# Kernel optimization log

Measured on AMD Instinct MI355X. Metric: run time of the kernel, lower is better.

The kernel has to match this reference:

```python
import jax, jax.numpy as jnp
import numpy as np

B, L, D, H = 2, 2048, 1024, 16
HD = D // H  # head_dim = 64


def setup_inputs() -> dict:
    key = jax.random.key(0)
    ks = jax.random.split(key, 8)
    queries = jax.random.normal(ks[0], (B, L, D), dtype=jnp.float32)
    keys = jax.random.normal(ks[1], (B, L, D), dtype=jnp.float32)
    values = jax.random.normal(ks[2], (B, L, D), dtype=jnp.float32)
    mask = jax.random.randint(ks[3], (B, L, L), 0, 2) > 0  # True = masked
    s = 1.0 / np.sqrt(D)
    W_q = jax.random.normal(ks[4], (D, D), dtype=jnp.float32) * s
    W_k = jax.random.normal(ks[5], (D, D), dtype=jnp.float32) * s
    W_v = jax.random.normal(ks[6], (D, D), dtype=jnp.float32) * s
    W_o = jax.random.normal(ks[7], (D, D), dtype=jnp.float32) * s
    return {"queries": queries, "keys": keys, "values": values,
            "W_q": W_q, "W_k": W_k, "W_v": W_v, "W_o": W_o, "mask": mask}


def _split_heads(x):
    # [B, L, D] -> [B, H, L, HD]
    return x.reshape(B, L, H, HD).transpose(0, 2, 1, 3)


def reference(queries, keys, values, W_q, W_k, W_v, W_o, mask):
    # Linear projections (nn.Linear: x @ W.T, no bias)
    q = _split_heads(queries @ W_q.T)   # [B,H,Lq,HD]
    k = _split_heads(keys @ W_k.T)      # [B,H,Lk,HD]
    v = _split_heads(values @ W_v.T)    # [B,H,Lk,HD]
    scores = jnp.einsum('bnqd,bnkd->bnqk', q, k) / np.sqrt(HD)
    scores = jnp.where(mask[:, None, :, :], -1e9, scores)
    attn = jax.nn.softmax(scores, axis=-1)
    ctx = jnp.einsum('bnqk,bnkd->bnqd', attn, v)
    ctx = ctx.transpose(0, 2, 1, 3).reshape(B, L, D)
    return ctx @ W_o.T  # dropout p=0.0 -> identity
```

## Files before the change

kernel.cpp:

```cpp
#include <hip/hip_runtime.h>
#include <hip/hip_bf16.h>

typedef __bf16 bf16;
typedef __attribute__((ext_vector_type(8))) __bf16 bf16x8;
typedef __attribute__((ext_vector_type(4))) __bf16 bf16x4;
typedef __attribute__((ext_vector_type(4))) float f32x4;

#define B_   2
#define L_   2048
#define D_   1024
#define H_   16
#define HD_  64

__device__ __forceinline__ float fast_exp2(float x) {
  float e; asm("v_exp_f32 %0, %1" : "=v"(e) : "v"(x)); return e;
}

__device__ __forceinline__ void gll16(const bf16* g, bf16* l) {
  __builtin_amdgcn_global_load_lds((const __attribute__((address_space(1))) void*)g,
                                   (__attribute__((address_space(3))) void*)l,
                                   16, 0, 0);
}

__global__ void detect_kernel(const unsigned short* __restrict__ q_u,
                              const unsigned char* __restrict__ m_u,
                              int* __restrict__ flags) {
  __shared__ int cnt, odd;
  if (threadIdx.x == 0) { cnt = 0; odd = 0; }
  __syncthreads();
  int c = 0, o = 0;
  for (int i = 0; i < 8; i++) {
    int idx = threadIdx.x * 8 + i;
    unsigned e = (q_u[idx] >> 7) & 0xFF;
    if (e >= 0x8F || (e > 0 && e <= 0x6F)) c++;
    if ((idx & 3) && m_u[idx]) o = 1;
  }
  atomicAdd(&cnt, c);
  if (o) atomicOr(&odd, 1);
  __syncthreads();
  if (threadIdx.x == 0) { flags[0] = (cnt > 128) ? 1 : 0; flags[1] = odd; }
}

__device__ __forceinline__ void canon_body(const void* src, bf16* dst, int i, int f) {
  if (f) {
    const float4* s = (const float4*)src;
    float4 a = s[i / 4], b2 = s[i / 4 + 1];
    bf16x8 o;
    o[0] = (bf16)a.x;  o[1] = (bf16)a.y;  o[2] = (bf16)a.z;  o[3] = (bf16)a.w;
    o[4] = (bf16)b2.x; o[5] = (bf16)b2.y; o[6] = (bf16)b2.z; o[7] = (bf16)b2.w;
    *(bf16x8*)(dst + i) = o;
  } else {
    *(bf16x8*)(dst + i) = ((const bf16x8*)src)[i / 8];
  }
}

__global__ __launch_bounds__(256) void canon_pack(
    const void* xq, const void* xk, const void* xv,
    const void* Wq, const void* Wk, const void* Wv, const void* Wo,
    const void* mp,
    bf16* cxq, bf16* cxk, bf16* cxv,
    bf16* cWq, bf16* cWk, bf16* cWv, bf16* cWo,
    unsigned* __restrict__ bitsT,
    const int* __restrict__ flags) {
  int t = blockIdx.x;
  if (t >= 8192) {
    int wid = (t - 8192) * 256 + threadIdx.x;
    unsigned v = 0;
    if (flags[1]) {
      const uchar4* p = (const uchar4*)mp;
#pragma unroll
      for (int c = 0; c < 8; c++) {
        uchar4 u = p[wid * 8 + c];
        v |= (u.x ? 1u : 0u) << (c * 4 + 0);
        v |= (u.y ? 1u : 0u) << (c * 4 + 1);
        v |= (u.z ? 1u : 0u) << (c * 4 + 2);
        v |= (u.w ? 1u : 0u) << (c * 4 + 3);
      }
    } else {
      const int4* p = (const int4*)mp;
#pragma unroll
      for (int c = 0; c < 8; c++) {
        int4 u = p[wid * 8 + c];
        v |= (u.x ? 1u : 0u) << (c * 4 + 0);
        v |= (u.y ? 1u : 0u) << (c * 4 + 1);
        v |= (u.z ? 1u : 0u) << (c * 4 + 2);
        v |= (u.w ? 1u : 0u) << (c * 4 + 3);
      }
    }
    int row = wid >> 6, word = wid & 63;
    int kt = word >> 1, half = word & 1;
    bitsT[((size_t)kt * 4096 + row) * 2 + half] = v;
    return;
  }
  const int f = flags[0];
  const void* src; bf16* dst; int base;
  if (t < 2048)      { src = xq; dst = cxq; base = t * 2048; }
  else if (t < 4096) { src = xk; dst = cxk; base = (t - 2048) * 2048; }
  else if (t < 6144) { src = xv; dst = cxv; base = (t - 4096) * 2048; }
  else {
    int w = t - 6144, wi = w >> 9;
    base = (w & 511) * 2048;
    if (wi == 0)      { src = Wq; dst = cWq; }
    else if (wi == 1) { src = Wk; dst = cWk; }
    else if (wi == 2) { src = Wv; dst = cWv; }
    else              { src = Wo; dst = cWo; }
  }
  canon_body(src, dst, base + threadIdx.x * 8, f);
}

__global__ __launch_bounds__(256) void gemm_qkv(
    const bf16* __restrict__ Aq, const bf16* __restrict__ Bq, bf16* __restrict__ Cq,
    const bf16* __restrict__ Ak, const bf16* __restrict__ Bk, bf16* __restrict__ Ck,
    const bf16* __restrict__ Av, const bf16* __restrict__ Bv, bf16* __restrict__ VT) {
  __shared__ bf16 smem[128 * 136];
  bf16* sA = smem;
  bf16* sB = smem + 4096;
  const int z = blockIdx.z;
  const bf16* A  = (z == 0) ? Aq : (z == 1) ? Ak : Av;
  const bf16* Bm = (z == 0) ? Bq : (z == 1) ? Bk : Bv;

  const int tid = threadIdx.x;
  const int w = tid >> 6, lane = tid & 63, qd = lane >> 4, r = lane & 15;
  const int wm = w >> 1, wn = w & 1;
  const int m0 = blockIdx.x * 128, n0 = blockIdx.y * 128;

  f32x4 acc[4][4];
#pragma unroll
  for (int i = 0; i < 4; i++)
#pragma unroll
    for (int j = 0; j < 4; j++) acc[i][j] = (f32x4){0.f, 0.f, 0.f, 0.f};

  for (int k0 = 0; k0 < 1024; k0 += 32) {
    __syncthreads();
#pragma unroll
    for (int p = 0; p < 2; p++) {
      int c = p * 256 + tid;
      gll16(A + (size_t)(m0 + (c >> 2)) * 1024 + k0 + (c & 3) * 8, sA + c * 8);
    }
#pragma unroll
    for (int p = 0; p < 2; p++) {
      int c = p * 256 + tid;
      gll16(Bm + (size_t)(n0 + (c >> 2)) * 1024 + k0 + (c & 3) * 8, sB + c * 8);
    }
    __syncthreads();
    bf16x8 af[4], bfv[4];
#pragma unroll
    for (int i = 0; i < 4; i++)
      af[i] = *(const bf16x8*)&sA[(wm * 64 + i * 16 + r) * 32 + qd * 8];
#pragma unroll
    for (int j = 0; j < 4; j++)
      bfv[j] = *(const bf16x8*)&sB[(wn * 64 + j * 16 + r) * 32 + qd * 8];
#pragma unroll
    for (int i = 0; i < 4; i++)
#pragma unroll
      for (int j = 0; j < 4; j++)
        acc[i][j] = __builtin_amdgcn_mfma_f32_16x16x32_bf16(af[i], bfv[j], acc[i][j], 0, 0, 0);
  }

  if (z < 2) {
    bf16* C = (z == 0) ? Cq : Ck;
    const float s = (z == 0) ? 0.1803368801f : 1.0f;
#pragma unroll
    for (int i = 0; i < 4; i++)
#pragma unroll
      for (int j = 0; j < 4; j++)
#pragma unroll
        for (int rr = 0; rr < 4; rr++) {
          int row = m0 + wm * 64 + i * 16 + qd * 4 + rr;
          int col = n0 + wn * 64 + j * 16 + r;
          C[(size_t)row * 1024 + col] = (bf16)(acc[i][j][rr] * s);
        }
  } else {
    __syncthreads();
#pragma unroll
    for (int i = 0; i < 4; i++)
#pragma unroll
      for (int j = 0; j < 4; j++) {
        int col = wn * 64 + j * 16 + r;
        int rowb = wm * 64 + i * 16 + qd * 4;
        bf16x4 v4;
#pragma unroll
        for (int rr = 0; rr < 4; rr++) v4[rr] = (bf16)acc[i][j][rr];
        *(bf16x4*)&smem[col * 136 + rowb] = v4;
      }
    __syncthreads();
    const int b = m0 >> 11, tok0 = m0 & 2047, h0 = n0 >> 6;
#pragma unroll
    for (int p = 0; p < 8; p++) {
      int c = p * 256 + tid;
      int dl = c >> 4, ch = c & 15;
      bf16x8 v = *(const bf16x8*)&smem[dl * 136 + ch * 8];
      int head = h0 + (dl >> 6), d = dl & 63;
      *(bf16x8*)(VT + ((size_t)((b * 16 + head) * 64 + d)) * 2048 + tok0 + ch * 8) = v;
    }
  }
}

__global__ __launch_bounds__(256) void gemm_nt_out(const bf16* __restrict__ A,
                                                   const bf16* __restrict__ Bm,
                                                   void* __restrict__ Cout,
                                                   const int* __restrict__ flags) {
  __shared__ bf16 sA[128 * 32];
  __shared__ bf16 sB[64 * 32];
  const int tid = threadIdx.x;
  const int w = tid >> 6, lane = tid & 63, qd = lane >> 4, r = lane & 15;
  const int wm = w >> 1, wn = w & 1;
  const int m0 = blockIdx.x * 128, n0 = blockIdx.y * 64;

  f32x4 acc[4][2];
#pragma unroll
  for (int i = 0; i < 4; i++)
#pragma unroll
    for (int j = 0; j < 2; j++) acc[i][j] = (f32x4){0.f, 0.f, 0.f, 0.f};

  for (int k0 = 0; k0 < 1024; k0 += 32) {
    __syncthreads();
    {
      int c0 = tid;
      gll16(A + (size_t)(m0 + (c0 >> 2)) * 1024 + k0 + (c0 & 3) * 8, sA + c0 * 8);
      int c1 = 256 + tid;
      gll16(A + (size_t)(m0 + (c1 >> 2)) * 1024 + k0 + (c1 & 3) * 8, sA + c1 * 8);
      int cb = tid;
      gll16(Bm + (size_t)(n0 + (cb >> 2)) * 1024 + k0 + (cb & 3) * 8, sB + cb * 8);
    }
    __syncthreads();
    bf16x8 af[4], bfv[2];
#pragma unroll
    for (int i = 0; i < 4; i++)
      af[i] = *(const bf16x8*)&sA[(wm * 64 + i * 16 + r) * 32 + qd * 8];
#pragma unroll
    for (int j = 0; j < 2; j++)
      bfv[j] = *(const bf16x8*)&sB[(wn * 32 + j * 16 + r) * 32 + qd * 8];
#pragma unroll
    for (int i = 0; i < 4; i++)
#pragma unroll
      for (int j = 0; j < 2; j++)
        acc[i][j] = __builtin_amdgcn_mfma_f32_16x16x32_bf16(af[i], bfv[j], acc[i][j], 0, 0, 0);
  }
  const int f = flags[0];
#pragma unroll
  for (int i = 0; i < 4; i++)
#pragma unroll
    for (int j = 0; j < 2; j++)
#pragma unroll
      for (int rr = 0; rr < 4; rr++) {
        int row = m0 + wm * 64 + i * 16 + qd * 4 + rr;
        int col = n0 + wn * 32 + j * 16 + r;
        if (f) ((float*)Cout)[(size_t)row * 1024 + col] = acc[i][j][rr];
        else   ((bf16*)Cout)[(size_t)row * 1024 + col] = (bf16)acc[i][j][rr];
      }
}

__global__ __launch_bounds__(256) void attn_kernel(const bf16* __restrict__ Q,
                                                   const bf16* __restrict__ Kp,
                                                   const bf16* __restrict__ Vt,
                                                   const unsigned* __restrict__ bitsT,
                                                   bf16* __restrict__ CTX) {
  __shared__ bf16 sK[2][64 * 64];
  __shared__ bf16 sVT[2][64 * 64];
  __shared__ bf16 sP[128 * 72];
  const int tid = threadIdx.x;
  const int w = tid >> 6, lane = tid & 63, qd = lane >> 4, r = lane & 15;
  const int wgid = blockIdx.x;
  const int bh = ((wgid >> 7) << 3) + (wgid & 7);
  const int b = bh >> 4, h = bh & 15;
  const int q0 = ((wgid >> 3) & 15) * 128;

  bf16x8 qf[2][2];
#pragma unroll
  for (int i = 0; i < 2; i++)
#pragma unroll
    for (int ks = 0; ks < 2; ks++)
      qf[i][ks] = *(const bf16x8*)(Q + (size_t)(b * L_ + q0 + w * 32 + i * 16 + r) * D_ +
                                   h * HD_ + ks * 32 + qd * 8);

  bf16x8 ones;
#pragma unroll
  for (int e = 0; e < 8; e++) ones[e] = (bf16)1.0f;

  f32x4 o[2][4], lacc[2];
#pragma unroll
  for (int i = 0; i < 2; i++) {
#pragma unroll
    for (int dj = 0; dj < 4; dj++) o[i][dj] = (f32x4){0.f, 0.f, 0.f, 0.f};
    lacc[i] = (f32x4){0.f, 0.f, 0.f, 0.f};
  }

#define STAGE_KV(KT, KB, VB)                                                        \
  {                                                                                 \
    _Pragma("unroll")                                                               \
    for (int p = 0; p < 2; p++) {                                                   \
      int c = p * 256 + tid;                                                        \
      int row = c >> 3, kc = c & 7;                                                 \
      int kcg = kc ^ (row & 7);                                                     \
      gll16(Kp + (size_t)(b * L_ + (KT) * 64 + row) * D_ + h * HD_ + kcg * 8,       \
            (KB) + c * 8);                                                          \
    }                                                                               \
    _Pragma("unroll")                                                               \
    for (int p = 0; p < 2; p++) {                                                   \
      int c = p * 256 + tid;                                                        \
      int row = c >> 3, kc = c & 7;                                                 \
      int kcg = kc ^ (row & 7);                                                     \
      gll16(Vt + (size_t)(bh * 64 + row) * L_ + (KT) * 64 + kcg * 8, (VB) + c * 8); \
    }                                                                               \
  }

#define MLOAD(KT, M0, M1)                                                                       \
  {                                                                                             \
    M0 = *(const uint2*)(bitsT + ((size_t)(KT) * 4096 + b * 2048 + q0 + w * 32 + r) * 2);       \
    M1 = *(const uint2*)(bitsT + ((size_t)(KT) * 4096 + b * 2048 + q0 + w * 32 + 16 + r) * 2);  \
  }

  STAGE_KV(0, &sK[0][0], &sVT[0][0]);
  uint2 mc0, mc1, mn0, mn1;
  MLOAD(0, mc0, mc1);
  mn0 = mc0; mn1 = mc1;

#pragma unroll 2
  for (int it = 0; it < 32; ++it) {
    const bf16* kb = &sK[it & 1][0];
    const bf16* vb = &sVT[it & 1][0];

    if (it < 31) {
      STAGE_KV(it + 1, &sK[(it + 1) & 1][0], &sVT[(it + 1) & 1][0]);
      MLOAD(it + 1, mn0, mn1);
      asm volatile("s_waitcnt vmcnt(6)" ::: "memory");
    } else {
      asm volatile("s_waitcnt vmcnt(0)" ::: "memory");
    }
    __builtin_amdgcn_sched_barrier(0);
    __builtin_amdgcn_s_barrier();

    bf16x8 kf[4][2];
#pragma unroll
    for (int j = 0; j < 4; j++)
#pragma unroll
      for (int ks = 0; ks < 2; ks++) {
        int row = j * 16 + r;
        int phys = (ks * 4 + qd) ^ (row & 7);
        kf[j][ks] = *(const bf16x8*)&kb[row * 64 + phys * 8];
      }

#pragma unroll
    for (int i = 0; i < 2; i++) {
      f32x4 S[4];
      __builtin_amdgcn_s_setprio(1);
#pragma unroll
      for (int j = 0; j < 4; j++) {
        S[j] = (f32x4){0.f, 0.f, 0.f, 0.f};
#pragma unroll
        for (int ks = 0; ks < 2; ks++)
          S[j] = __builtin_amdgcn_mfma_f32_16x16x32_bf16(kf[j][ks], qf[i][ks], S[j], 0, 0, 0);
      }
      __builtin_amdgcn_s_setprio(0);
      const uint2 m64 = (i == 0) ? mc0 : mc1;
#pragma unroll
      for (int j = 0; j < 4; j++) {
        unsigned word = (j < 2) ? m64.x : m64.y;
        unsigned nib = (word >> ((j & 1) * 16 + qd * 4)) & 0xFu;
        bf16x4 pv;
#pragma unroll
        for (int rr = 0; rr < 4; rr++) {
          float e = fast_exp2(S[j][rr]);
          pv[rr] = (bf16)(((nib >> rr) & 1u) ? 0.f : e);
        }
        *(bf16x4*)&sP[(w * 32 + i * 16 + r) * 72 + j * 16 + qd * 4] = pv;
      }
    }
    asm volatile("s_waitcnt lgkmcnt(0)" ::: "memory");

    bf16x8 vf[4][2];
#pragma unroll
    for (int dj = 0; dj < 4; dj++)
#pragma unroll
      for (int ks = 0; ks < 2; ks++) {
        int row = dj * 16 + r;
        int phys = (ks * 4 + qd) ^ (row & 7);
        vf[dj][ks] = *(const bf16x8*)&vb[row * 64 + phys * 8];
      }
    __builtin_amdgcn_s_setprio(1);
#pragma unroll
    for (int i = 0; i < 2; i++)
#pragma unroll
      for (int ks = 0; ks < 2; ks++) {
        bf16x8 pf = *(const bf16x8*)&sP[(w * 32 + i * 16 + r) * 72 + ks * 32 + qd * 8];
#pragma unroll
        for (int dj = 0; dj < 4; dj++)
          o[i][dj] = __builtin_amdgcn_mfma_f32_16x16x32_bf16(pf, vf[dj][ks], o[i][dj], 0, 0, 0);
        lacc[i] = __builtin_amdgcn_mfma_f32_16x16x32_bf16(pf, ones, lacc[i], 0, 0, 0);
      }
    __builtin_amdgcn_s_setprio(0);

    __builtin_amdgcn_s_barrier();
    mc0 = mn0; mc1 = mn1;
  }
#undef STAGE_KV
#undef MLOAD

#pragma unroll
  for (int i = 0; i < 2; i++) {
    float inv[4];
#pragma unroll
    for (int rr = 0; rr < 4; rr++) inv[rr] = 1.0f / lacc[i][rr];
#pragma unroll
    for (int dj = 0; dj < 4; dj++)
#pragma unroll
      for (int rr = 0; rr < 4; rr++) {
        int rg = b * L_ + q0 + w * 32 + i * 16 + qd * 4 + rr;
        int col = h * HD_ + dj * 16 + r;
        CTX[(size_t)rg * 1024 + col] = (bf16)(o[i][dj][rr] * inv[rr]);
      }
  }
}

extern "C" void kernel_launch(void* const* d_in, const int* in_sizes, int n_in,
                              void* d_out, int out_size, void* d_ws, size_t ws_size,
                              hipStream_t stream) {
  const void* xq = d_in[0];
  const void* xk = d_in[1];
  const void* xv = d_in[2];
  const void* Wq = d_in[3];
  const void* Wk = d_in[4];
  const void* Wv = d_in[5];
  const void* Wo = d_in[6];
  const void* mask = d_in[7];

  char* ws = (char*)d_ws;
  const size_t MB = 1048576;
  int*      FLAGS = (int*)(ws + 0);
  unsigned* BITS  = (unsigned*)(ws + 4096);
  bf16* cWo = (bf16*)(ws + 2 * MB);
  bf16* cWq = (bf16*)(ws + 4 * MB);
  bf16* cWk = (bf16*)(ws + 6 * MB);
  bf16* cWv = (bf16*)(ws + 8 * MB);
  bf16* cxq = (bf16*)(ws + 10 * MB);
  bf16* cxk = (bf16*)(ws + 18 * MB);
  bf16* cxv = (bf16*)(ws + 26 * MB);
  bf16* Q   = (bf16*)(ws + 34 * MB);
  bf16* K   = (bf16*)(ws + 42 * MB);
  bf16* VT  = (bf16*)(ws + 50 * MB);
  bf16* CTX = (bf16*)(ws + 26 * MB);

  detect_kernel<<<1, 256, 0, stream>>>((const unsigned short*)xq,
                                       (const unsigned char*)mask, FLAGS);
  canon_pack<<<9216, 256, 0, stream>>>(xq, xk, xv, Wq, Wk, Wv, Wo, mask,
                                       cxq, cxk, cxv, cWq, cWk, cWv, cWo,
                                       BITS, FLAGS);
  gemm_qkv<<<dim3(32, 8, 3), 256, 0, stream>>>(cxq, cWq, Q,
                                               cxk, cWk, K,
                                               cxv, cWv, VT);
  attn_kernel<<<512, 256, 0, stream>>>(Q, K, VT, BITS, CTX);
  gemm_nt_out<<<dim3(32, 16), 256, 0, stream>>>(CTX, cWo, d_out, FLAGS);
}
```

Measured before the change: 261.5 us.

## Split attention query tile across eight waves with sixteen rows each

The attention block grows from 4 to 8 wavefronts, and each wave now owns 16 query rows instead of 32. K/V staging is spread over 512 threads, so each thread issues one load per tensor per tile, and the vmcnt wait is adjusted to match. This halves per-wave accumulator registers and doubles the waves available to hide latency. The cost is that every wave reloads the same K and V fragments from LDS for half as much MFMA work, and there are more barrier participants.

Result: faster. 253.3 us (-3.1%).

```diff
diff --git a/kernel.cpp b/kernel.cpp
--- a/kernel.cpp
+++ b/kernel.cpp
@@ -251,11 +251,11 @@
       }
 }
 
-__global__ __launch_bounds__(256) void attn_kernel(const bf16* __restrict__ Q,
-                                                   const bf16* __restrict__ Kp,
-                                                   const bf16* __restrict__ Vt,
-                                                   const unsigned* __restrict__ bitsT,
-                                                   bf16* __restrict__ CTX) {
+__global__ __launch_bounds__(512, 4) void attn_kernel(const bf16* __restrict__ Q,
+                                                      const bf16* __restrict__ Kp,
+                                                      const bf16* __restrict__ Vt,
+                                                      const unsigned* __restrict__ bitsT,
+                                                      bf16* __restrict__ CTX) {
   __shared__ bf16 sK[2][64 * 64];
   __shared__ bf16 sVT[2][64 * 64];
   __shared__ bf16 sP[128 * 72];
@@ -265,56 +265,39 @@
   const int bh = ((wgid >> 7) << 3) + (wgid & 7);
   const int b = bh >> 4, h = bh & 15;
   const int q0 = ((wgid >> 3) & 15) * 128;
-
-  bf16x8 qf[2][2];
-#pragma unroll
-  for (int i = 0; i < 2; i++)
-#pragma unroll
-    for (int ks = 0; ks < 2; ks++)
-      qf[i][ks] = *(const bf16x8*)(Q + (size_t)(b * L_ + q0 + w * 32 + i * 16 + r) * D_ +
-                                   h * HD_ + ks * 32 + qd * 8);
+  const int qrow = w * 16 + r;
+
+  bf16x8 qf[2];
+#pragma unroll
+  for (int ks = 0; ks < 2; ks++)
+    qf[ks] = *(const bf16x8*)(Q + (size_t)(b * L_ + q0 + qrow) * D_ +
+                              h * HD_ + ks * 32 + qd * 8);
 
   bf16x8 ones;
 #pragma unroll
   for (int e = 0; e < 8; e++) ones[e] = (bf16)1.0f;
 
-  f32x4 o[2][4], lacc[2];
-#pragma unroll
-  for (int i = 0; i < 2; i++) {
-#pragma unroll
-    for (int dj = 0; dj < 4; dj++) o[i][dj] = (f32x4){0.f, 0.f, 0.f, 0.f};
-    lacc[i] = (f32x4){0.f, 0.f, 0.f, 0.f};
-  }
-
-#define STAGE_KV(KT, KB, VB)                                                        \
-  {                                                                                 \
-    _Pragma("unroll")                                                               \
-    for (int p = 0; p < 2; p++) {                                                   \
-      int c = p * 256 + tid;                                                        \
-      int row = c >> 3, kc = c & 7;                                                 \
-      int kcg = kc ^ (row & 7);                                                     \
-      gll16(Kp + (size_t)(b * L_ + (KT) * 64 + row) * D_ + h * HD_ + kcg * 8,       \
-            (KB) + c * 8);                                                          \
-    }                                                                               \
-    _Pragma("unroll")                                                               \
-    for (int p = 0; p < 2; p++) {                                                   \
-      int c = p * 256 + tid;                                                        \
-      int row = c >> 3, kc = c & 7;                                                 \
-      int kcg = kc ^ (row & 7);                                                     \
-      gll16(Vt + (size_t)(bh * 64 + row) * L_ + (KT) * 64 + kcg * 8, (VB) + c * 8); \
-    }                                                                               \
-  }
-
-#define MLOAD(KT, M0, M1)                                                                       \
-  {                                                                                             \
-    M0 = *(const uint2*)(bitsT + ((size_t)(KT) * 4096 + b * 2048 + q0 + w * 32 + r) * 2);       \
-    M1 = *(const uint2*)(bitsT + ((size_t)(KT) * 4096 + b * 2048 + q0 + w * 32 + 16 + r) * 2);  \
-  }
+  f32x4 o[4], lacc;
+#pragma unroll
+  for (int dj = 0; dj < 4; dj++) o[dj] = (f32x4){0.f, 0.f, 0.f, 0.f};
+  lacc = (f32x4){0.f, 0.f, 0.f, 0.f};
+
+#define STAGE_KV(KT, KB, VB)                                                      \
+  {                                                                               \
+    int row = tid >> 3, kc = tid & 7;                                             \
+    int kcg = kc ^ (row & 7);                                                     \
+    gll16(Kp + (size_t)(b * L_ + (KT) * 64 + row) * D_ + h * HD_ + kcg * 8,       \
+          (KB) + tid * 8);                                                        \
+    gll16(Vt + (size_t)(bh * 64 + row) * L_ + (KT) * 64 + kcg * 8, (VB) + tid * 8); \
+  }
+
+#define MLOAD(KT, M0)                                                             \
+  M0 = *(const uint2*)(bitsT + ((size_t)(KT) * 4096 + b * 2048 + q0 + qrow) * 2);
 
   STAGE_KV(0, &sK[0][0], &sVT[0][0]);
-  uint2 mc0, mc1, mn0, mn1;
-  MLOAD(0, mc0, mc1);
-  mn0 = mc0; mn1 = mc1;
+  uint2 mc, mn;
+  MLOAD(0, mc);
+  mn = mc;
 
 #pragma unroll 2
   for (int it = 0; it < 32; ++it) {
@@ -323,8 +306,8 @@
 
     if (it < 31) {
       STAGE_KV(it + 1, &sK[(it + 1) & 1][0], &sVT[(it + 1) & 1][0]);
-      MLOAD(it + 1, mn0, mn1);
-      asm volatile("s_waitcnt vmcnt(6)" ::: "memory");
+      MLOAD(it + 1, mn);
+      asm volatile("s_waitcnt vmcnt(3)" ::: "memory");
     } else {
       asm volatile("s_waitcnt vmcnt(0)" ::: "memory");
     }
@@ -341,8 +324,7 @@
         kf[j][ks] = *(const bf16x8*)&kb[row * 64 + phys * 8];
       }
 
-#pragma unroll
-    for (int i = 0; i < 2; i++) {
+    {
       f32x4 S[4];
       __builtin_amdgcn_s_setprio(1);
 #pragma unroll
@@ -350,13 +332,12 @@
         S[j] = (f32x4){0.f, 0.f, 0.f, 0.f};
 #pragma unroll
         for (int ks = 0; ks < 2; ks++)
-          S[j] = __builtin_amdgcn_mfma_f32_16x16x32_bf16(kf[j][ks], qf[i][ks], S[j], 0, 0, 0);
+          S[j] = __builtin_amdgcn_mfma_f32_16x16x32_bf16(kf[j][ks], qf[ks], S[j], 0, 0, 0);
       }
       __builtin_amdgcn_s_setprio(0);
-      const uint2 m64 = (i == 0) ? mc0 : mc1;
 #pragma unroll
       for (int j = 0; j < 4; j++) {
-        unsigned word = (j < 2) ? m64.x : m64.y;
+        unsigned word = (j < 2) ? mc.x : mc.y;
         unsigned nib = (word >> ((j & 1) * 16 + qd * 4)) & 0xFu;
         bf16x4 pv;
 #pragma unroll
@@ -364,7 +345,7 @@
           float e = fast_exp2(S[j][rr]);
           pv[rr] = (bf16)(((nib >> rr) & 1u) ? 0.f : e);
         }
-        *(bf16x4*)&sP[(w * 32 + i * 16 + r) * 72 + j * 16 + qd * 4] = pv;
+        *(bf16x4*)&sP[qrow * 72 + j * 16 + qd * 4] = pv;
       }
     }
     asm volatile("s_waitcnt lgkmcnt(0)" ::: "memory");
@@ -380,35 +361,32 @@
       }
     __builtin_amdgcn_s_setprio(1);
 #pragma unroll
-    for (int i = 0; i < 2; i++)
-#pragma unroll
-      for (int ks = 0; ks < 2; ks++) {
-        bf16x8 pf = *(const bf16x8*)&sP[(w * 32 + i * 16 + r) * 72 + ks * 32 + qd * 8];
-#pragma unroll
-        for (int dj = 0; dj < 4; dj++)
-          o[i][dj] = __builtin_amdgcn_mfma_f32_16x16x32_bf16(pf, vf[dj][ks], o[i][dj], 0, 0, 0);
-        lacc[i] = __builtin_amdgcn_mfma_f32_16x16x32_bf16(pf, ones, lacc[i], 0, 0, 0);
-      }
+    for (int ks = 0; ks < 2; ks++) {
+      bf16x8 pf = *(const bf16x8*)&sP[qrow * 72 + ks * 32 + qd * 8];
+#pragma unroll
+      for (int dj = 0; dj < 4; dj++)
+        o[dj] = __builtin_amdgcn_mfma_f32_16x16x32_bf16(pf, vf[dj][ks], o[dj], 0, 0, 0);
+      lacc = __builtin_amdgcn_mfma_f32_16x16x32_bf16(pf, ones, lacc, 0, 0, 0);
+    }
     __builtin_amdgcn_s_setprio(0);
 
     __builtin_amdgcn_s_barrier();
-    mc0 = mn0; mc1 = mn1;
+    mc = mn;
   }
 #undef STAGE_KV
 #undef MLOAD
 
-#pragma unroll
-  for (int i = 0; i < 2; i++) {
+  {
     float inv[4];
 #pragma unroll
-    for (int rr = 0; rr < 4; rr++) inv[rr] = 1.0f / lacc[i][rr];
+    for (int rr = 0; rr < 4; rr++) inv[rr] = 1.0f / lacc[rr];
 #pragma unroll
     for (int dj = 0; dj < 4; dj++)
 #pragma unroll
       for (int rr = 0; rr < 4; rr++) {
-        int rg = b * L_ + q0 + w * 32 + i * 16 + qd * 4 + rr;
+        int rg = b * L_ + q0 + w * 16 + qd * 4 + rr;
         int col = h * HD_ + dj * 16 + r;
-        CTX[(size_t)rg * 1024 + col] = (bf16)(o[i][dj][rr] * inv[rr]);
+        CTX[(size_t)rg * 1024 + col] = (bf16)(o[dj][rr] * inv[rr]);
       }
   }
 }
@@ -449,6 +427,6 @@
   gemm_qkv<<<dim3(32, 8, 3), 256, 0, stream>>>(cxq, cWq, Q,
                                                cxk, cWk, K,
                                                cxv, cWv, VT);
-  attn_kernel<<<512, 256, 0, stream>>>(Q, K, VT, BITS, CTX);
+  attn_kernel<<<512, 512, 0, stream>>>(Q, K, VT, BITS, CTX);
   gemm_nt_out<<<dim3(32, 16), 256, 0, stream>>>(CTX, cWo, d_out, FLAGS);
 }
```
